# Performance work log

Measured on AMD Instinct MI355X. Metric: run time of the kernel, lower is better.

## Reference

```python
import jax, jax.numpy as jnp
import numpy as np
import math

B, L, C, H = 2, 2048, 1024, 16
D = C // H
MAX_SCALE_MUL = math.log(100.0)
EPS = 1e-12  # F.normalize eps


def setup_inputs() -> dict:
    key = jax.random.key(0)
    ks = jax.random.split(key, 6)
    x = jax.random.normal(ks[0], (B, L, C), dtype=jnp.float32)
    attn_bias = jax.random.normal(ks[1], (1, 1, L, L), dtype=jnp.float32) * 0.02
    w_qkv = jax.random.normal(ks[2], (3 * C, C), dtype=jnp.float32) * (1.0 / math.sqrt(C))
    q_bias = jnp.zeros((C,), dtype=jnp.float32)
    v_bias = jnp.zeros((C,), dtype=jnp.float32)
    scale_mul = jnp.full((1, H, 1, 1), math.log(4.0), dtype=jnp.float32)
    w_proj = jax.random.normal(ks[3], (C, C), dtype=jnp.float32) * (1.0 / math.sqrt(C))
    b_proj = jnp.zeros((C,), dtype=jnp.float32)
    return {"x": x, "attn_bias": attn_bias, "w_qkv": w_qkv, "q_bias": q_bias,
            "v_bias": v_bias, "scale_mul": scale_mul, "w_proj": w_proj, "b_proj": b_proj}


def _l2norm(t):
    # matches F.normalize(dim=-1): x / max(||x||, eps)
    n = jnp.sqrt(jnp.sum(t * t, axis=-1, keepdims=True))
    return t / jnp.maximum(n, EPS)


def reference(x, attn_bias, w_qkv, q_bias, v_bias, scale_mul, w_proj, b_proj):
    b, l, c = x.shape
    bias = jnp.concatenate([q_bias, jnp.zeros_like(q_bias), v_bias])  # [3C]
    qkv = x @ w_qkv.T + bias                              # [B,L,3C]
    qkv = qkv.reshape(b, l, 3, H, D)
    qkv = jnp.transpose(qkv, (2, 0, 3, 1, 4))             # [3,B,H,L,D]
    q, k, v = qkv[0], qkv[1], qkv[2]
    # attn_l2_norm path: scale = 1, learned per-head multiplier on normalized q
    sm = jnp.exp(jnp.minimum(scale_mul, MAX_SCALE_MUL))   # [1,H,1,1]
    q = _l2norm(q) * sm
    k = _l2norm(k)
    scores = jnp.einsum('bhld,bhmd->bhlm', q, k) + attn_bias  # [B,H,L,L]
    attn = jax.nn.softmax(scores, axis=-1)
    oup = jnp.einsum('bhlm,bhmd->bhld', attn, v)          # [B,H,L,D]
    oup = jnp.transpose(oup, (0, 2, 1, 3)).reshape(b, l, c)
    return oup @ w_proj.T + b_proj
```

## Files before the change

kernel.cpp:

```cpp
#include <hip/hip_runtime.h>

typedef __attribute__((ext_vector_type(8))) short short8v;
typedef __attribute__((ext_vector_type(4))) float f32x4;
typedef __attribute__((ext_vector_type(16))) float f32x16;
typedef __attribute__((ext_vector_type(4))) int int4v;
typedef __attribute__((ext_vector_type(4))) unsigned int uint4v;
typedef __attribute__((ext_vector_type(4))) unsigned short u16x4;

#define MFMA16(a, b, c) __builtin_amdgcn_mfma_f32_16x16x32_bf16(a, b, c, 0, 0, 0)
#define MFMA32(a, b, c) __builtin_amdgcn_mfma_f32_32x32x16_bf16(a, b, c, 0, 0, 0)

__device__ __forceinline__ unsigned short f2bf(float f) {
  unsigned int u = __builtin_bit_cast(unsigned int, f);
  return (unsigned short)((u + 0x7FFFu + ((u >> 16) & 1u)) >> 16);
}
__device__ __forceinline__ float bf2f(unsigned short s) {
  return __builtin_bit_cast(float, (unsigned int)s << 16);
}
__device__ __forceinline__ float exp2_hw(float x) {
  float r;
  asm("v_exp_f32 %0, %1" : "=v"(r) : "v"(x));
  return r;
}
__device__ __forceinline__ void gl_lds16(const unsigned short* g, unsigned short* l) {
  __builtin_amdgcn_global_load_lds(
      (const __attribute__((address_space(1))) void*)g,
      (__attribute__((address_space(3))) void*)l, 16, 0, 0);
}

__global__ __launch_bounds__(256) void cast_all(
    const float* __restrict__ x, const float* __restrict__ wqkv,
    const float* __restrict__ wproj, const float* __restrict__ ab,
    unsigned short* __restrict__ xb, unsigned short* __restrict__ wqkvb,
    unsigned short* __restrict__ wprojb, unsigned short* __restrict__ biasb) {
  int i = blockIdx.x * 256 + threadIdx.x;
  const float* src;
  unsigned short* dst;
  int off;
  float scale = 1.0f;
  if (i < 1048576) { src = x; dst = xb; off = i; }
  else if (i < 1835008) { src = wqkv; dst = wqkvb; off = i - 1048576; }
  else if (i < 2097152) { src = wproj; dst = wprojb; off = i - 1835008; }
  else { src = ab; dst = biasb; off = i - 2097152; scale = 1.44269504088896f; }
  f32x4 v = *(const f32x4*)(src + (size_t)off * 4);
  u16x4 o;
#pragma unroll
  for (int j = 0; j < 4; ++j) o[j] = f2bf(v[j] * scale);
  *(u16x4*)(dst + (size_t)off * 4) = o;
}

__global__ __launch_bounds__(256) void gemm_qkv(
    const unsigned short* __restrict__ A, const unsigned short* __restrict__ Bm,
    unsigned short* __restrict__ qn, unsigned short* __restrict__ kn,
    unsigned short* __restrict__ vt,
    const float* __restrict__ bias_q, const float* __restrict__ bias_v,
    const float* __restrict__ scale_mul) {
  __shared__ unsigned short Ssl[16384];
  unsigned short* Asl = Ssl;
  unsigned short* Bsl = Ssl + 8192;
  const int tid = threadIdx.x;
  const int lane = tid & 63;
  const int wave = tid >> 6;
  const int wr = wave >> 1, wc = wave & 1;
  const int c = lane & 15, g = lane >> 4;
  const int rowBase = blockIdx.x * 128;
  const int colBase = blockIdx.y * 128;
  const int srow = lane >> 3, scol = (lane & 7) * 8;

  f32x4 acc[4][4];
#pragma unroll
  for (int m = 0; m < 4; ++m)
#pragma unroll
    for (int n = 0; n < 4; ++n) acc[m][n] = (f32x4){0.f, 0.f, 0.f, 0.f};

  for (int k0 = 0; k0 < 1024; k0 += 64) {
#pragma unroll
    for (int it = 0; it < 4; ++it) {
      int ci = wave * 4 + it;
      int r = ci * 8 + srow;
      gl_lds16(A + (size_t)(rowBase + r) * 1024 + k0 + scol, &Asl[ci * 512]);
      gl_lds16(Bm + (size_t)(colBase + r) * 1024 + k0 + scol, &Bsl[ci * 512]);
    }
    __syncthreads();
#pragma unroll
    for (int kk = 0; kk < 2; ++kk) {
      short8v af[4], bfr[4];
#pragma unroll
      for (int m = 0; m < 4; ++m)
        af[m] = *(const short8v*)&Asl[(wr * 64 + m * 16 + c) * 64 + kk * 32 + g * 8];
#pragma unroll
      for (int n = 0; n < 4; ++n)
        bfr[n] = *(const short8v*)&Bsl[(wc * 64 + n * 16 + c) * 64 + kk * 32 + g * 8];
#pragma unroll
      for (int m = 0; m < 4; ++m)
#pragma unroll
        for (int n = 0; n < 4; ++n) acc[m][n] = MFMA16(af[m], bfr[n], acc[m][n]);
    }
    __syncthreads();
  }

  const int sec = colBase >> 10;
  const int jbase = (colBase & 1023) + wc * 64;
  const int headCol = jbase >> 6;

  if (sec == 2) {
    unsigned short* tls = Ssl + wave * 4096;
#pragma unroll
    for (int m = 0; m < 4; ++m)
#pragma unroll
      for (int r = 0; r < 4; ++r)
#pragma unroll
        for (int n = 0; n < 4; ++n) {
          int d = n * 16 + c;
          int ll = m * 16 + g * 4 + r;
          tls[d * 64 + (ll ^ ((d & 7) << 3))] =
              f2bf(acc[m][n][r] + bias_v[jbase + n * 16 + c]);
        }
    __syncthreads();
    const int b = rowBase >> 11;
    const int bhh = b * 16 + headCol;
    const int lbase = (rowBase & 2047) + wr * 64;
#pragma unroll
    for (int j = 0; j < 8; ++j) {
      int idx = j * 64 + lane;
      int d = idx >> 3;
      int l8 = (idx & 7) * 8;
      short8v v8 = *(const short8v*)&tls[d * 64 + (l8 ^ ((d & 7) << 3))];
      *(short8v*)(vt + ((size_t)(bhh * 64 + d)) * 2048 + lbase + l8) = v8;
    }
  } else {
    float qsc = 1.0f;
    if (sec == 0)
      qsc = __expf(fminf(scale_mul[headCol], 4.605170185988091f)) * 1.44269504088896f;
#pragma unroll
    for (int m = 0; m < 4; ++m) {
#pragma unroll
      for (int r = 0; r < 4; ++r) {
        float vv[4];
#pragma unroll
        for (int n = 0; n < 4; ++n) {
          int jn = jbase + n * 16 + c;
          float bias = (sec == 0) ? bias_q[jn] : 0.0f;
          vv[n] = acc[m][n][r] + bias;
        }
        float ss = vv[0] * vv[0] + vv[1] * vv[1] + vv[2] * vv[2] + vv[3] * vv[3];
        ss += __shfl_xor(ss, 1);
        ss += __shfl_xor(ss, 2);
        ss += __shfl_xor(ss, 4);
        ss += __shfl_xor(ss, 8);
        float sc = qsc / fmaxf(sqrtf(ss), 1e-12f);
        int grow = rowBase + wr * 64 + m * 16 + g * 4 + r;
        int bb = grow >> 11, l = grow & 2047;
        int bhh = bb * 16 + headCol;
#pragma unroll
        for (int n = 0; n < 4; ++n) {
          int d = n * 16 + c;
          unsigned short o = f2bf(vv[n] * sc);
          if (sec == 0)
            qn[(bhh * 2048 + l) * 64 + d] = o;
          else
            kn[(bhh * 2048 + l) * 64 + d] = o;
        }
      }
    }
  }
}

__global__ __launch_bounds__(256) void gemm_proj(
    const unsigned short* __restrict__ A, const unsigned short* __restrict__ Bm,
    float* __restrict__ outf, const float* __restrict__ bias) {
  __shared__ unsigned short Asl[64 * 64];
  __shared__ unsigned short Bsl[64 * 64];
  const int tid = threadIdx.x;
  const int lane = tid & 63;
  const int wave = tid >> 6;
  const int wr = wave >> 1, wc = wave & 1;
  const int c = lane & 15, g = lane >> 4;
  const int rowBase = blockIdx.x * 64;
  const int colBase = blockIdx.y * 64;
  const int srow = lane >> 3, scol = (lane & 7) * 8;

  f32x4 acc[2][2];
#pragma unroll
  for (int m = 0; m < 2; ++m)
#pragma unroll
    for (int n = 0; n < 2; ++n) acc[m][n] = (f32x4){0.f, 0.f, 0.f, 0.f};

  for (int k0 = 0; k0 < 1024; k0 += 64) {
#pragma unroll
    for (int it = 0; it < 2; ++it) {
      int ci = wave * 2 + it;
      int r = ci * 8 + srow;
      gl_lds16(A + (size_t)(rowBase + r) * 1024 + k0 + scol, &Asl[ci * 512]);
      gl_lds16(Bm + (size_t)(colBase + r) * 1024 + k0 + scol, &Bsl[ci * 512]);
    }
    __syncthreads();
#pragma unroll
    for (int kk = 0; kk < 2; ++kk) {
      short8v af[2], bfr[2];
#pragma unroll
      for (int m = 0; m < 2; ++m)
        af[m] = *(const short8v*)&Asl[(wr * 32 + m * 16 + c) * 64 + kk * 32 + g * 8];
#pragma unroll
      for (int n = 0; n < 2; ++n)
        bfr[n] = *(const short8v*)&Bsl[(wc * 32 + n * 16 + c) * 64 + kk * 32 + g * 8];
#pragma unroll
      for (int m = 0; m < 2; ++m)
#pragma unroll
        for (int n = 0; n < 2; ++n) acc[m][n] = MFMA16(af[m], bfr[n], acc[m][n]);
    }
    __syncthreads();
  }

#pragma unroll
  for (int m = 0; m < 2; ++m)
#pragma unroll
    for (int n = 0; n < 2; ++n)
#pragma unroll
      for (int r = 0; r < 4; ++r) {
        int grow = rowBase + wr * 32 + m * 16 + g * 4 + r;
        int gcol = colBase + wc * 32 + n * 16 + c;
        outf[(size_t)grow * 1024 + gcol] = acc[m][n][r] + bias[gcol];
      }
}

__global__ __launch_bounds__(256) void attn_fwd(
    const unsigned short* __restrict__ qn, const unsigned short* __restrict__ kn,
    const unsigned short* __restrict__ vt, const unsigned short* __restrict__ biasb,
    unsigned short* __restrict__ oup) {
  __shared__ unsigned short Ksl[2][128][72];
  __shared__ unsigned short Vsl[2][64][136];
  const int tid = threadIdx.x;
  const int lane = tid & 63;
  const int wave = tid >> 6;
  const int c5 = lane & 31;
  const int h = lane >> 5;
  const int qt = blockIdx.x;
  const int bh = blockIdx.y;
  const int b = bh >> 4, hd = bh & 15;
  const int q = qt * 128 + wave * 32 + c5;

  short8v qf[4];
  {
    const unsigned short* qp = qn + ((size_t)bh * 2048 + q) * 64 + h * 8;
#pragma unroll
    for (int kd = 0; kd < 4; ++kd) qf[kd] = *(const short8v*)(qp + kd * 16);
  }
  const unsigned short* kb = kn + (size_t)bh * 131072;
  const unsigned short* vb = vt + (size_t)bh * 131072;
  const unsigned short* bq = biasb + (size_t)q * 2048 + h * 4;

  int rk[4], ck[4], rv[4], cv[4];
#pragma unroll
  for (int i = 0; i < 4; ++i) {
    int flat = tid * 8 + i * 2048;
    rk[i] = flat >> 6;  ck[i] = flat & 63;
    rv[i] = flat >> 7;  cv[i] = flat & 127;
  }

  int4v kreg[4], vreg[4];
  u16x4 bb[4][4];

  auto ISSUE = [&](int kt) {
#pragma unroll
    for (int i = 0; i < 4; ++i) {
      kreg[i] = *(const int4v*)(kb + (size_t)(kt * 128 + rk[i]) * 64 + ck[i]);
      vreg[i] = *(const int4v*)(vb + (size_t)rv[i] * 2048 + kt * 128 + cv[i]);
    }
  };
  auto ISSUEB = [&](int n, int kt) {
#pragma unroll
    for (int Qd = 0; Qd < 4; ++Qd)
      bb[n][Qd] = *(const u16x4*)(bq + kt * 128 + n * 32 + Qd * 8);
  };
  auto WRITE = [&](int buf) {
#pragma unroll
    for (int i = 0; i < 4; ++i) {
      *(int4v*)&Ksl[buf][rk[i]][ck[i]] = kreg[i];
      *(int4v*)&Vsl[buf][rv[i]][cv[i]] = vreg[i];
    }
  };

  float l_run = 0.0f;
  f32x16 o0 = {}, o1 = {};

  ISSUE(0);
#pragma unroll
  for (int n = 0; n < 4; ++n) ISSUEB(n, 0);
  WRITE(0);
  __syncthreads();

  for (int kt = 0; kt < 16; ++kt) {
    const int cur = kt & 1;
    const bool more = (kt + 1) < 16;
    if (more) ISSUE(kt + 1);
    float rs = 0.0f;

#pragma unroll
    for (int n = 0; n < 4; ++n) {
      f32x16 s;
#pragma unroll
      for (int Qd = 0; Qd < 4; ++Qd)
#pragma unroll
        for (int r = 0; r < 4; ++r) s[Qd * 4 + r] = bf2f(bb[n][Qd][r]);
      if (more) ISSUEB(n, kt + 1);

      __builtin_amdgcn_s_setprio(1);
#pragma unroll
      for (int kd = 0; kd < 4; ++kd) {
        short8v kf = *(const short8v*)&Ksl[cur][n * 32 + c5][kd * 16 + h * 8];
        s = MFMA32(kf, qf[kd], s);
      }
      __builtin_amdgcn_s_setprio(0);

#pragma unroll
      for (int e = 0; e < 16; ++e) {
        float p = exp2_hw(s[e]);
        s[e] = p;
        rs += p;
      }

      unsigned int w[4][2];
#pragma unroll
      for (int Qd = 0; Qd < 4; ++Qd) {
        asm("v_cvt_pk_bf16_f32 %0, %1, %2"
            : "=v"(w[Qd][0]) : "v"(s[Qd * 4 + 0]), "v"(s[Qd * 4 + 1]));
        asm("v_cvt_pk_bf16_f32 %0, %1, %2"
            : "=v"(w[Qd][1]) : "v"(s[Qd * 4 + 2]), "v"(s[Qd * 4 + 3]));
      }

      __builtin_amdgcn_s_setprio(1);
#pragma unroll
      for (int kc = 0; kc < 2; ++kc) {
        unsigned int W[4];
#pragma unroll
        for (int u = 0; u < 2; ++u) {
          unsigned int A = w[kc * 2][u];
          unsigned int B = w[kc * 2 + 1][u];
          unsigned int pub = h ? A : B;
          unsigned int ex = (unsigned int)__shfl_xor((int)pub, 32);
          W[u] = h ? ex : A;
          W[2 + u] = h ? B : ex;
        }
        uint4v wv = {W[0], W[1], W[2], W[3]};
        short8v pa = __builtin_bit_cast(short8v, wv);
        short8v v0 = *(const short8v*)&Vsl[cur][c5][n * 32 + kc * 16 + h * 8];
        short8v v1 = *(const short8v*)&Vsl[cur][32 + c5][n * 32 + kc * 16 + h * 8];
        o0 = MFMA32(pa, v0, o0);
        o1 = MFMA32(pa, v1, o1);
      }
      __builtin_amdgcn_s_setprio(0);
    }

    rs += __shfl_xor(rs, 32);
    l_run += rs;

    if (more) WRITE(cur ^ 1);
    __syncthreads();
  }

  float linv = 1.0f / l_run;
#pragma unroll
  for (int e = 0; e < 16; ++e) {
    int ql = (e & 3) + 8 * (e >> 2) + 4 * h;
    float inv = __shfl(linv, ql);
    int grow = b * 2048 + qt * 128 + wave * 32 + ql;
    oup[(size_t)grow * 1024 + hd * 64 + c5] = f2bf(o0[e] * inv);
    oup[(size_t)grow * 1024 + hd * 64 + 32 + c5] = f2bf(o1[e] * inv);
  }
}

extern "C" void kernel_launch(void* const* d_in, const int* in_sizes, int n_in,
                              void* d_out, int out_size, void* d_ws, size_t ws_size,
                              hipStream_t stream) {
  const float* x = (const float*)d_in[0];
  const float* attn_bias = (const float*)d_in[1];
  const float* w_qkv = (const float*)d_in[2];
  const float* q_bias = (const float*)d_in[3];
  const float* v_bias = (const float*)d_in[4];
  const float* scale_mul = (const float*)d_in[5];
  const float* w_proj = (const float*)d_in[6];
  const float* b_proj = (const float*)d_in[7];
  float* out = (float*)d_out;

  char* ws = (char*)d_ws;
  unsigned short* xb = (unsigned short*)(ws);
  unsigned short* oup = (unsigned short*)(ws);
  unsigned short* wqkvb = (unsigned short*)(ws + (8 << 20));
  unsigned short* wprojb = (unsigned short*)(ws + (14 << 20));
  unsigned short* biasb = (unsigned short*)(ws + (16 << 20));
  unsigned short* qn = (unsigned short*)(ws + (24 << 20));
  unsigned short* kn = (unsigned short*)(ws + (32 << 20));
  unsigned short* vt = (unsigned short*)(ws + (40 << 20));

  cast_all<<<12288, 256, 0, stream>>>(x, w_qkv, w_proj, attn_bias, xb, wqkvb,
                                      wprojb, biasb);
  gemm_qkv<<<dim3(32, 24), 256, 0, stream>>>(xb, wqkvb, qn, kn, vt, q_bias,
                                             v_bias, scale_mul);
  attn_fwd<<<dim3(16, 32), 256, 0, stream>>>(qn, kn, vt, biasb, oup);
  gemm_proj<<<dim3(64, 16), 256, 0, stream>>>(oup, wprojb, out, b_proj);
}
```

Baseline: 165.3 us.

## Rewrite QKV GEMM as 256x256 tile with double-buffered LDS prefetch

The QKV projection GEMM moves from 128x128 tiles with 4 waves to 256x256 tiles with 8 waves. It double-buffers the A/B tiles in LDS and issues the next k-tile's global-to-LDS loads in quarters between MFMA sub-blocks, gated by explicit vmcnt waits, barriers and s_setprio. The goal is to hide global load latency and raise data reuse per block. In exchange it uses 128KB of LDS and launches only 192 blocks, which can leave CUs idle on a 256-CU part, and it depends on exact waitcnt accounting to stay correct.

```diff
diff --git a/kernel.cpp b/kernel.cpp
--- a/kernel.cpp
+++ b/kernel.cpp
@@ -49,91 +49,182 @@
   *(u16x4*)(dst + (size_t)off * 4) = o;
 }
 
-__global__ __launch_bounds__(256) void gemm_qkv(
+__global__ __launch_bounds__(512) void gemm_qkv(
     const unsigned short* __restrict__ A, const unsigned short* __restrict__ Bm,
     unsigned short* __restrict__ qn, unsigned short* __restrict__ kn,
     unsigned short* __restrict__ vt,
     const float* __restrict__ bias_q, const float* __restrict__ bias_v,
     const float* __restrict__ scale_mul) {
-  __shared__ unsigned short Ssl[16384];
-  unsigned short* Asl = Ssl;
-  unsigned short* Bsl = Ssl + 8192;
+  __shared__ unsigned short Al[2][16384];
+  __shared__ unsigned short Bl[2][16384];
   const int tid = threadIdx.x;
   const int lane = tid & 63;
   const int wave = tid >> 6;
-  const int wr = wave >> 1, wc = wave & 1;
+  const int wr = wave >> 2;
+  const int wcn = wave & 3;
   const int c = lane & 15, g = lane >> 4;
-  const int rowBase = blockIdx.x * 128;
-  const int colBase = blockIdx.y * 128;
-  const int srow = lane >> 3, scol = (lane & 7) * 8;
-
-  f32x4 acc[4][4];
-#pragma unroll
-  for (int m = 0; m < 4; ++m)
+  const int rowBase = blockIdx.x * 256;
+  const int colBase = blockIdx.y * 256;
+  const int srow = tid >> 3;
+  const int scol = (tid & 7) * 8;
+
+  auto STAGE_A = [&](int kt, int half) {
+    int slot = kt & 1;
+#pragma unroll
+    for (int rr = 0; rr < 2; ++rr) {
+      int r = half * 2 + rr;
+      gl_lds16(A + (size_t)(rowBase + r * 64 + srow) * 1024 + kt * 64 + scol,
+               &Al[slot][r * 4096 + wave * 512]);
+    }
+  };
+  auto STAGE_B = [&](int kt, int half) {
+    int slot = kt & 1;
+#pragma unroll
+    for (int rr = 0; rr < 2; ++rr) {
+      int r = half * 2 + rr;
+      gl_lds16(Bm + (size_t)(colBase + r * 64 + srow) * 1024 + kt * 64 + scol,
+               &Bl[slot][r * 4096 + wave * 512]);
+    }
+  };
+
+  f32x4 acc[8][4];
+#pragma unroll
+  for (int m = 0; m < 8; ++m)
 #pragma unroll
     for (int n = 0; n < 4; ++n) acc[m][n] = (f32x4){0.f, 0.f, 0.f, 0.f};
 
-  for (int k0 = 0; k0 < 1024; k0 += 64) {
-#pragma unroll
-    for (int it = 0; it < 4; ++it) {
-      int ci = wave * 4 + it;
-      int r = ci * 8 + srow;
-      gl_lds16(A + (size_t)(rowBase + r) * 1024 + k0 + scol, &Asl[ci * 512]);
-      gl_lds16(Bm + (size_t)(colBase + r) * 1024 + k0 + scol, &Bsl[ci * 512]);
-    }
+  short8v af[4][2];
+  short8v bf[2][2];
+
+  STAGE_A(0, 0);
+  STAGE_B(0, 0);
+  STAGE_B(0, 1);
+  STAGE_A(0, 1);
+
+  for (int kt = 0; kt < 16; ++kt) {
+    const int slot = kt & 1;
+    const bool more = (kt + 1) < 16;
+
+    __builtin_amdgcn_s_barrier();
+    if (more) STAGE_A(kt + 1, 0);
+    if (more) asm volatile("s_waitcnt vmcnt(4)" ::: "memory");
+    else      asm volatile("s_waitcnt vmcnt(2)" ::: "memory");
+    __builtin_amdgcn_s_barrier();
+#pragma unroll
+    for (int mm = 0; mm < 4; ++mm)
+#pragma unroll
+      for (int kk = 0; kk < 2; ++kk)
+        af[mm][kk] = *(const short8v*)
+            &Al[slot][(wr * 128 + mm * 16 + c) * 64 + kk * 32 + g * 8];
+#pragma unroll
+    for (int nn = 0; nn < 2; ++nn)
+#pragma unroll
+      for (int kk = 0; kk < 2; ++kk)
+        bf[nn][kk] = *(const short8v*)
+            &Bl[slot][(wcn * 64 + nn * 16 + c) * 64 + kk * 32 + g * 8];
+    __builtin_amdgcn_s_setprio(1);
+#pragma unroll
+    for (int mm = 0; mm < 4; ++mm)
+#pragma unroll
+      for (int nn = 0; nn < 2; ++nn)
+#pragma unroll
+        for (int kk = 0; kk < 2; ++kk)
+          acc[mm][nn] = MFMA16(af[mm][kk], bf[nn][kk], acc[mm][nn]);
+    __builtin_amdgcn_s_setprio(0);
+
+    if (more) STAGE_B(kt + 1, 0);
+#pragma unroll
+    for (int nn = 0; nn < 2; ++nn)
+#pragma unroll
+      for (int kk = 0; kk < 2; ++kk)
+        bf[nn][kk] = *(const short8v*)
+            &Bl[slot][(wcn * 64 + (2 + nn) * 16 + c) * 64 + kk * 32 + g * 8];
+    __builtin_amdgcn_s_setprio(1);
+#pragma unroll
+    for (int mm = 0; mm < 4; ++mm)
+#pragma unroll
+      for (int nn = 0; nn < 2; ++nn)
+#pragma unroll
+        for (int kk = 0; kk < 2; ++kk)
+          acc[mm][2 + nn] = MFMA16(af[mm][kk], bf[nn][kk], acc[mm][2 + nn]);
+    __builtin_amdgcn_s_setprio(0);
+
+    if (more) STAGE_B(kt + 1, 1);
+    if (more) asm volatile("s_waitcnt vmcnt(6)" ::: "memory");
+    else      asm volatile("s_waitcnt vmcnt(0)" ::: "memory");
+    __builtin_amdgcn_s_barrier();
+#pragma unroll
+    for (int mm = 0; mm < 4; ++mm)
+#pragma unroll
+      for (int kk = 0; kk < 2; ++kk)
+        af[mm][kk] = *(const short8v*)
+            &Al[slot][(wr * 128 + (4 + mm) * 16 + c) * 64 + kk * 32 + g * 8];
+    __builtin_amdgcn_s_setprio(1);
+#pragma unroll
+    for (int mm = 0; mm < 4; ++mm)
+#pragma unroll
+      for (int nn = 0; nn < 2; ++nn)
+#pragma unroll
+        for (int kk = 0; kk < 2; ++kk)
+          acc[4 + mm][2 + nn] = MFMA16(af[mm][kk], bf[nn][kk], acc[4 + mm][2 + nn]);
+    __builtin_amdgcn_s_setprio(0);
+
+    if (more) STAGE_A(kt + 1, 1);
+#pragma unroll
+    for (int nn = 0; nn < 2; ++nn)
+#pragma unroll
+      for (int kk = 0; kk < 2; ++kk)
+        bf[nn][kk] = *(const short8v*)
+            &Bl[slot][(wcn * 64 + nn * 16 + c) * 64 + kk * 32 + g * 8];
+    __builtin_amdgcn_s_setprio(1);
+#pragma unroll
+    for (int mm = 0; mm < 4; ++mm)
+#pragma unroll
+      for (int nn = 0; nn < 2; ++nn)
+#pragma unroll
+        for (int kk = 0; kk < 2; ++kk)
+          acc[4 + mm][nn] = MFMA16(af[mm][kk], bf[nn][kk], acc[4 + mm][nn]);
+    __builtin_amdgcn_s_setprio(0);
+  }
+
+  const int sec = colBase >> 10;
+  const int jbase = (colBase & 1023) + wcn * 64;
+  const int headCol = jbase >> 6;
+  const int bI = rowBase >> 11;
+  const int bhh = bI * 16 + headCol;
+
+  if (sec == 2) {
     __syncthreads();
-#pragma unroll
-    for (int kk = 0; kk < 2; ++kk) {
-      short8v af[4], bfr[4];
-#pragma unroll
-      for (int m = 0; m < 4; ++m)
-        af[m] = *(const short8v*)&Asl[(wr * 64 + m * 16 + c) * 64 + kk * 32 + g * 8];
-#pragma unroll
-      for (int n = 0; n < 4; ++n)
-        bfr[n] = *(const short8v*)&Bsl[(wc * 64 + n * 16 + c) * 64 + kk * 32 + g * 8];
-#pragma unroll
-      for (int m = 0; m < 4; ++m)
-#pragma unroll
-        for (int n = 0; n < 4; ++n) acc[m][n] = MFMA16(af[m], bfr[n], acc[m][n]);
-    }
-    __syncthreads();
-  }
-
-  const int sec = colBase >> 10;
-  const int jbase = (colBase & 1023) + wc * 64;
-  const int headCol = jbase >> 6;
-
-  if (sec == 2) {
-    unsigned short* tls = Ssl + wave * 4096;
-#pragma unroll
-    for (int m = 0; m < 4; ++m)
-#pragma unroll
-      for (int r = 0; r < 4; ++r)
-#pragma unroll
-        for (int n = 0; n < 4; ++n) {
-          int d = n * 16 + c;
-          int ll = m * 16 + g * 4 + r;
-          tls[d * 64 + (ll ^ ((d & 7) << 3))] =
-              f2bf(acc[m][n][r] + bias_v[jbase + n * 16 + c]);
-        }
-    __syncthreads();
-    const int b = rowBase >> 11;
-    const int bhh = b * 16 + headCol;
-    const int lbase = (rowBase & 2047) + wr * 64;
-#pragma unroll
-    for (int j = 0; j < 8; ++j) {
-      int idx = j * 64 + lane;
-      int d = idx >> 3;
-      int l8 = (idx & 7) * 8;
-      short8v v8 = *(const short8v*)&tls[d * 64 + (l8 ^ ((d & 7) << 3))];
-      *(short8v*)(vt + ((size_t)(bhh * 64 + d)) * 2048 + lbase + l8) = v8;
+    unsigned short* tls = &Al[0][0] + wave * 4096;
+#pragma unroll
+    for (int lh = 0; lh < 2; ++lh) {
+      const int lbase = (rowBase & 2047) + wr * 128 + lh * 64;
+#pragma unroll
+      for (int mq = 0; mq < 4; ++mq)
+#pragma unroll
+        for (int r = 0; r < 4; ++r)
+#pragma unroll
+          for (int n = 0; n < 4; ++n) {
+            int d = n * 16 + c;
+            int ll = mq * 16 + g * 4 + r;
+            tls[d * 64 + (ll ^ ((d & 7) << 3))] =
+                f2bf(acc[lh * 4 + mq][n][r] + bias_v[jbase + n * 16 + c]);
+          }
+#pragma unroll
+      for (int j = 0; j < 8; ++j) {
+        int idx = j * 64 + lane;
+        int d = idx >> 3;
+        int l8 = (idx & 7) * 8;
+        short8v v8 = *(const short8v*)&tls[d * 64 + (l8 ^ ((d & 7) << 3))];
+        *(short8v*)(vt + ((size_t)(bhh * 64 + d)) * 2048 + lbase + l8) = v8;
+      }
     }
   } else {
     float qsc = 1.0f;
     if (sec == 0)
       qsc = __expf(fminf(scale_mul[headCol], 4.605170185988091f)) * 1.44269504088896f;
 #pragma unroll
-    for (int m = 0; m < 4; ++m) {
+    for (int m = 0; m < 8; ++m) {
 #pragma unroll
       for (int r = 0; r < 4; ++r) {
         float vv[4];
@@ -149,9 +240,8 @@
         ss += __shfl_xor(ss, 4);
         ss += __shfl_xor(ss, 8);
         float sc = qsc / fmaxf(sqrtf(ss), 1e-12f);
-        int grow = rowBase + wr * 64 + m * 16 + g * 4 + r;
-        int bb = grow >> 11, l = grow & 2047;
-        int bhh = bb * 16 + headCol;
+        int grow = rowBase + wr * 128 + m * 16 + g * 4 + r;
+        int l = grow & 2047;
 #pragma unroll
         for (int n = 0; n < 4; ++n) {
           int d = n * 16 + c;
@@ -395,7 +485,7 @@
 
   cast_all<<<12288, 256, 0, stream>>>(x, w_qkv, w_proj, attn_bias, xb, wqkvb,
                                       wprojb, biasb);
-  gemm_qkv<<<dim3(32, 24), 256, 0, stream>>>(xb, wqkvb, qn, kn, vt, q_bias,
+  gemm_qkv<<<dim3(16, 12), 512, 0, stream>>>(xb, wqkvb, qn, kn, vt, q_bias,
                                              v_bias, scale_mul);
   attn_fwd<<<dim3(16, 32), 256, 0, stream>>>(qn, kn, vt, biasb, oup);
   gemm_proj<<<dim3(64, 16), 256, 0, stream>>>(oup, wprojb, out, b_proj);
```

New measurement: 167.1 us. No clear change (+1.1%).
